# Performance work log

Hardware: AMD Instinct MI355X
Metric: run time of the kernel (lower is better)

The kernel has to match this reference:

```python
import jax, jax.numpy as jnp
import numpy as np

WIN = 5  # mask_window_size


def gather_windows(indices, image, win):
    """Gather win x win windows of pixel features centered at each query index.
    indices: [Q, 2] (y, x) int; image: [H, W, F].
    Returns keys [Q, win, win, F] (zeros at out-of-bounds) and pad mask [Q, win, win]."""
    H, W = image.shape[0], image.shape[1]
    offs = jnp.arange(win) - win // 2
    yy = (indices[:, 0, None] + offs)[:, :, None]
    xx = (indices[:, 1, None] + offs)[:, None, :]
    pad = (yy < 0) | (yy >= H) | (xx < 0) | (xx >= W)
    yc = jnp.clip(yy, 0, H - 1)
    xc = jnp.clip(xx, 0, W - 1)
    keys = image[yc, xc]
    keys = jnp.where(pad[..., None], jnp.zeros((), keys.dtype), keys)
    return keys, pad


def mlp(x, w1, b1, w2, b2):
    return jax.nn.relu(x @ w1 + b1) @ w2 + b2


def setup_inputs() -> dict:
    key = jax.random.key(0)
    ks = jax.random.split(key, 8)
    Q, Dq, F, Hd = 16384, 128, 128, 256
    H, W = 1024, 1024
    return {
        "queries": jax.random.normal(ks[0], (Q, Dq), jnp.float32),
        "query_indices": jax.random.randint(ks[1], (Q, 2), 0, H),
        "image": jax.random.normal(ks[2], (H, W, F), jnp.float32),
        "pm_w1": jax.random.normal(ks[3], (F, Hd), jnp.float32) * 0.02,
        "pm_b1": jnp.zeros((Hd,), jnp.float32),
        "pm_w2": jax.random.normal(ks[4], (Hd, Dq), jnp.float32) * 0.02,
        "pm_b2": jnp.zeros((Dq,), jnp.float32),
        "qp_w1": jax.random.normal(ks[5], (Dq, Hd), jnp.float32) * 0.02,
        "qp_b1": jnp.zeros((Hd,), jnp.float32),
        "qp_w2": jax.random.normal(ks[6], (Hd, F), jnp.float32) * 0.02,
        "qp_b2": jnp.zeros((F,), jnp.float32),
    }


def reference(queries, query_indices, image, pm_w1, pm_b1, pm_w2, pm_b2,
              qp_w1, qp_b1, qp_w2, qp_b2):
    # windowed key gather with out-of-bounds padding
    mask_keys, key_pad_mask = gather_windows(query_indices, image, WIN)  # [Q,w,w,F]
    # pixel_mask_head on gathered keys: F -> hidden -> query_dim
    mlped_mask_keys = mlp(mask_keys, pm_w1, pm_b1, pm_w2, pm_b2)          # [Q,w,w,Dq]
    binary_mask_logits = jnp.einsum('qf,qhwf->qhw', queries, mlped_mask_keys)
    # query_portion_head on queries: query_dim -> hidden -> F
    mlped_queries = mlp(queries, qp_w1, qp_b1, qp_w2, qp_b2)              # [Q,F]
    portion_logits = jnp.einsum('qf,qhwf->qhw', mlped_queries, mask_keys)
    # additive -inf pad bias (matches masked_fill + add in torch)
    pad_bias = jnp.where(key_pad_mask, -jnp.inf, 0.0).astype(binary_mask_logits.dtype)
    binary_mask_logits = binary_mask_logits + pad_bias
    portion_logits = portion_logits + pad_bias
    nonzero_key_mask = jnp.any(mask_keys != 0, axis=-1)
    return binary_mask_logits, portion_logits, nonzero_key_mask
```

## Files before the change

### kernel.cpp

```cpp
#include <hip/hip_runtime.h>
#include <math.h>

#define NEG_SENTINEL (-3.0e38f)


typedef __bf16 bf16_t;
typedef __bf16 bf16x8 __attribute__((ext_vector_type(8)));
typedef float  f32x4  __attribute__((ext_vector_type(4)));

#define MFMA(a, b, c) __builtin_amdgcn_mfma_f32_16x16x32_bf16((a), (b), (c), 0, 0, 0)

__device__ inline bf16x8 cvt_bf16x8(float4 a, float4 b) {
  bf16x8 r;
  r[0] = (bf16_t)a.x; r[1] = (bf16_t)a.y; r[2] = (bf16_t)a.z; r[3] = (bf16_t)a.w;
  r[4] = (bf16_t)b.x; r[5] = (bf16_t)b.y; r[6] = (bf16_t)b.z; r[7] = (bf16_t)b.w;
  return r;
}

__global__ __launch_bounds__(256) void prep_kernel(
    const float* __restrict__ pm_w1, const float* __restrict__ qp_w1,
    const float* __restrict__ qp_w2, const float* __restrict__ pm_w2,
    bf16_t* __restrict__ w1t, bf16_t* __restrict__ qw1t,
    bf16_t* __restrict__ qw2t, bf16_t* __restrict__ w2pm)
{
  int i = blockIdx.x * 256 + threadIdx.x;
  int m = i >> 15, e = i & 32767;
  if (m == 0)      { int n = e >> 7, k = e & 127; w1t[e]  = (bf16_t)pm_w1[k * 256 + n]; }
  else if (m == 1) { int n = e >> 7, k = e & 127; qw1t[e] = (bf16_t)qp_w1[k * 256 + n]; }
  else if (m == 2) { int f = e >> 8, h = e & 255; qw2t[e] = (bf16_t)qp_w2[h * 128 + f]; }
  else             { w2pm[e] = (bf16_t)pm_w2[e]; }
}

__global__ __launch_bounds__(256) void query_side_kernel(
    const float* __restrict__ queries,
    const float* __restrict__ pm_b2,
    const float* __restrict__ qp_b1, const float* __restrict__ qp_b2,
    const bf16_t* __restrict__ qw1t, const bf16_t* __restrict__ w2pm,
    const bf16_t* __restrict__ qw2t,
    bf16_t* __restrict__ v_ws, bf16_t* __restrict__ mq_ws, float* __restrict__ c_ws)
{
  __shared__ float qb1_lds[256];
  __shared__ float qb2_lds[128];
  __shared__ __align__(16) bf16_t hq_lds[4][4096];

  const int t = threadIdx.x;
  const int w = t >> 6, l = t & 63, lr = l & 15, lg = l >> 4;
  const int qb = blockIdx.x * 64;
  const int qrow = qb + w * 16 + lr;

  for (int i = t; i < 256; i += 256) qb1_lds[i] = qp_b1[i];
  if (t < 128) qb2_lds[t] = qp_b2[t];

  bf16x8 aq[4];
  float cpart = 0.f;
  const float* qp = queries + (size_t)qrow * 128;
  #pragma unroll
  for (int s = 0; s < 4; ++s) {
    int k0 = s * 32 + lg * 8;
    float4 u0 = *(const float4*)(qp + k0);
    float4 u1 = *(const float4*)(qp + k0 + 4);
    float4 b0 = *(const float4*)(pm_b2 + k0);
    float4 b1 = *(const float4*)(pm_b2 + k0 + 4);
    cpart += u0.x*b0.x + u0.y*b0.y + u0.z*b0.z + u0.w*b0.w
           + u1.x*b1.x + u1.y*b1.y + u1.z*b1.z + u1.w*b1.w;
    aq[s] = cvt_bf16x8(u0, u1);
  }
  cpart += __shfl_xor(cpart, 16);
  cpart += __shfl_xor(cpart, 32);
  if (l < 16) c_ws[qb + w * 16 + l] = cpart;

  __syncthreads();

  bf16_t* hqw = hq_lds[w];

  #pragma unroll 2
  for (int n = 0; n < 16; ++n) {
    f32x4 aa = {0.f, 0.f, 0.f, 0.f};
    f32x4 ac = {0.f, 0.f, 0.f, 0.f};
    const int col = n * 16 + lr;
    #pragma unroll
    for (int s = 0; s < 4; ++s) {
      bf16x8 ba = *(const bf16x8*)(qw1t + (size_t)col * 128 + (s * 4 + lg) * 8);
      bf16x8 bc = *(const bf16x8*)(w2pm + (size_t)col * 128 + (s * 4 + lg) * 8);
      aa = MFMA(aq[s], ba, aa);
      ac = MFMA(aq[s], bc, ac);
    }
    float bv = qb1_lds[col];
    const int k8 = col >> 3;
    #pragma unroll
    for (int j = 0; j < 4; ++j) {
      int rw = lg * 4 + j;
      float hv = fmaxf(aa[j] + bv, 0.f);
      hqw[rw * 256 + ((k8 ^ rw) * 8) + (col & 7)] = (bf16_t)hv;
      v_ws[(size_t)(qb + w * 16 + rw) * 256 + col] = (bf16_t)ac[j];
    }
  }

  __syncthreads();

  bf16x8 ah[8];
  #pragma unroll
  for (int s = 0; s < 8; ++s)
    ah[s] = *(const bf16x8*)(hqw + lr * 256 + (((s * 4 + lg) ^ lr) * 8));
  #pragma unroll 2
  for (int n = 0; n < 8; ++n) {
    f32x4 am = {0.f, 0.f, 0.f, 0.f};
    const int col = n * 16 + lr;
    #pragma unroll
    for (int s = 0; s < 8; ++s) {
      bf16x8 bm = *(const bf16x8*)(qw2t + (size_t)col * 256 + (s * 4 + lg) * 8);
      am = MFMA(ah[s], bm, am);
    }
    float bv = qb2_lds[col];
    #pragma unroll
    for (int j = 0; j < 4; ++j)
      mq_ws[(size_t)(qb + w * 16 + lg * 4 + j) * 128 + col] = (bf16_t)(am[j] + bv);
  }
}

__global__ __launch_bounds__(320, 2) void window_kernel(
    const int* __restrict__ qidx, const float* __restrict__ image,
    const float* __restrict__ pm_b1,
    const bf16_t* __restrict__ w1t_g,
    const bf16_t* __restrict__ v_ws, const bf16_t* __restrict__ mq_ws,
    const float* __restrict__ c_ws, float* __restrict__ out, int Q)
{
  __shared__ __align__(16) bf16x8 w1t_lds[4096];
  __shared__ __align__(16) float v_lds[16 * 256];
  __shared__ __align__(16) float mq_lds[16 * 128];
  __shared__ float b1_lds[256];
  __shared__ float c_lds[16];
  __shared__ unsigned char pad_lds[400];

  const int t = threadIdx.x;
  const int w = t >> 6, l = t & 63, lr = l & 15, lg = l >> 4;
  const int qb = blockIdx.x * 16;

  bf16x8 afr[5][4];
  int aq[5], apad[5], nzf[5];
  #pragma unroll
  for (int tt = 0; tt < 5; ++tt) {
    int r = w * 80 + tt * 16 + lr;
    int ql = r / 25;
    int cell = r - ql * 25;
    int dy = cell / 5 - 2;
    int dx = cell - (dy + 2) * 5 - 2;
    int yy = qidx[2 * (qb + ql) + 0] + dy;
    int xx = qidx[2 * (qb + ql) + 1] + dx;
    bool pad = (yy < 0) | (yy >= 1024) | (xx < 0) | (xx >= 1024);
    aq[tt] = ql; apad[tt] = pad ? 1 : 0;
    if (l < 16) pad_lds[r] = (unsigned char)(pad ? 1 : 0);
    const float* px = image + (size_t)(pad ? 0 : (yy * 1024 + xx)) * 128;
    int nz = 0;
    #pragma unroll
    for (int s = 0; s < 4; ++s) {
      float4 u0 = make_float4(0.f, 0.f, 0.f, 0.f), u1 = u0;
      if (!pad) {
        u0 = *(const float4*)(px + s * 32 + lg * 8);
        u1 = *(const float4*)(px + s * 32 + lg * 8 + 4);
      }
      nz |= (u0.x != 0.f) | (u0.y != 0.f) | (u0.z != 0.f) | (u0.w != 0.f)
          | (u1.x != 0.f) | (u1.y != 0.f) | (u1.z != 0.f) | (u1.w != 0.f);
      afr[tt][s] = cvt_bf16x8(u0, u1);
    }
    nzf[tt] = nz;
  }

  {
    const bf16x8* wg = (const bf16x8*)w1t_g;
    for (int i = t; i < 4096; i += 320) {
      int row = i >> 4, k8 = i & 15;
      w1t_lds[(row << 4) | (k8 ^ (row & 15))] = wg[i];
    }
  }
  {
    const bf16_t* vg = v_ws + (size_t)qb * 256;
    for (int i = t; i < 512; i += 320) {
      bf16x8 d = *(const bf16x8*)(vg + i * 8);
      float4 lo = make_float4((float)d[0], (float)d[1], (float)d[2], (float)d[3]);
      float4 hi = make_float4((float)d[4], (float)d[5], (float)d[6], (float)d[7]);
      *(float4*)(v_lds + i * 8) = lo;
      *(float4*)(v_lds + i * 8 + 4) = hi;
    }
  }
  {
    const bf16_t* mg = mq_ws + (size_t)qb * 128;
    for (int i = t; i < 256; i += 320) {
      bf16x8 d = *(const bf16x8*)(mg + i * 8);
      float4 lo = make_float4((float)d[0], (float)d[1], (float)d[2], (float)d[3]);
      float4 hi = make_float4((float)d[4], (float)d[5], (float)d[6], (float)d[7]);
      *(float4*)(mq_lds + i * 8) = lo;
      *(float4*)(mq_lds + i * 8 + 4) = hi;
    }
  }
  for (int i = t; i < 256; i += 320) b1_lds[i] = pm_b1[i];
  if (t < 16) c_lds[t] = c_ws[qb + t];

  __syncthreads();

  #pragma unroll
  for (int tt = 0; tt < 5; ++tt) {
    const float* mrow = mq_lds + aq[tt] * 128;
    float pp = 0.f;
    #pragma unroll
    for (int s = 0; s < 4; ++s) {
      const float* m = mrow + s * 32 + lg * 8;
      float4 m0 = *(const float4*)(m);
      float4 m1 = *(const float4*)(m + 4);
      bf16x8 a = afr[tt][s];
      pp += (float)a[0]*m0.x + (float)a[1]*m0.y + (float)a[2]*m0.z + (float)a[3]*m0.w
          + (float)a[4]*m1.x + (float)a[5]*m1.y + (float)a[6]*m1.z + (float)a[7]*m1.w;
    }
    pp += __shfl_xor(pp, 16);
    pp += __shfl_xor(pp, 32);
    int nz = nzf[tt];
    nz |= __shfl_xor(nz, 16);
    nz |= __shfl_xor(nz, 32);
    if (l < 16) {
      int r = w * 80 + tt * 16 + l;
      int ql = aq[tt];
      int cell = r - ql * 25;
      int q = qb + ql;
      out[(size_t)Q * 25 + (size_t)q * 25 + cell]     = apad[tt] ? NEG_SENTINEL : pp;
      out[(size_t)2 * Q * 25 + (size_t)q * 25 + cell] = nz ? 1.0f : 0.0f;
    }
  }

  #pragma unroll
  for (int tt = 0; tt < 5; ++tt) {
    int rcq[4], rcell[4], vb[4], pc[4];
    #pragma unroll
    for (int j = 0; j < 4; ++j) {
      int rc = w * 80 + tt * 16 + lg * 4 + j;
      int q = rc / 25;
      rcq[j] = q; rcell[j] = rc - q * 25;
      pc[j] = pad_lds[rc];
      vb[j] = q * 256 + lr;
    }
    float part[4] = {0.f, 0.f, 0.f, 0.f};
    #pragma unroll 2
    for (int n = 0; n < 16; ++n) {
      f32x4 acc = {0.f, 0.f, 0.f, 0.f};
      #pragma unroll
      for (int s = 0; s < 4; ++s) {
        bf16x8 b = w1t_lds[((n * 16 + lr) << 4) | ((s * 4 + lg) ^ lr)];
        acc = MFMA(afr[tt][s], b, acc);
      }
      float bv = b1_lds[n * 16 + lr];
      #pragma unroll
      for (int j = 0; j < 4; ++j) {
        float hv = fmaxf(acc[j] + bv, 0.f);
        part[j] = fmaf(hv, v_lds[vb[j] + n * 16], part[j]);
      }
    }
    #pragma unroll
    for (int j = 0; j < 4; ++j) {
      float s = part[j];
      s += __shfl_xor(s, 1);
      s += __shfl_xor(s, 2);
      s += __shfl_xor(s, 4);
      s += __shfl_xor(s, 8);
      if (lr == 0)
        out[(size_t)(qb + rcq[j]) * 25 + rcell[j]] =
            pc[j] ? NEG_SENTINEL : (s + c_lds[rcq[j]]);
    }
  }
}

extern "C" void kernel_launch(void* const* d_in, const int* in_sizes, int n_in,
                              void* d_out, int out_size, void* d_ws, size_t ws_size,
                              hipStream_t stream) {
  const float* queries = (const float*)d_in[0];
  const int*   qidx    = (const int*)d_in[1];
  const float* image   = (const float*)d_in[2];
  const float* pm_w1   = (const float*)d_in[3];
  const float* pm_b1   = (const float*)d_in[4];
  const float* pm_w2   = (const float*)d_in[5];
  const float* pm_b2   = (const float*)d_in[6];
  const float* qp_w1   = (const float*)d_in[7];
  const float* qp_b1   = (const float*)d_in[8];
  const float* qp_w2   = (const float*)d_in[9];
  const float* qp_b2   = (const float*)d_in[10];
  float* out = (float*)d_out;

  const int Q = in_sizes[0] / 128;

  char* ws = (char*)d_ws;
  bf16_t* v_ws  = (bf16_t*)ws;  ws += (size_t)Q * 256 * 2;
  bf16_t* mq_ws = (bf16_t*)ws;  ws += (size_t)Q * 128 * 2;
  float*  c_ws  = (float*)ws;   ws += (size_t)Q * 4;
  bf16_t* w1t   = (bf16_t*)ws;  ws += 32768 * 2;
  bf16_t* qw1t  = (bf16_t*)ws;  ws += 32768 * 2;
  bf16_t* qw2t  = (bf16_t*)ws;  ws += 32768 * 2;
  bf16_t* w2pm  = (bf16_t*)ws;  ws += 32768 * 2;

  prep_kernel<<<512, 256, 0, stream>>>(pm_w1, qp_w1, qp_w2, pm_w2,
                                       w1t, qw1t, qw2t, w2pm);
  query_side_kernel<<<Q / 64, 256, 0, stream>>>(queries, pm_b2, qp_b1, qp_b2,
                                                qw1t, w2pm, qw2t, v_ws, mq_ws, c_ws);
  window_kernel<<<Q / 16, 320, 0, stream>>>(qidx, image, pm_b1, w1t,
                                            v_ws, mq_ws, c_ws, out, Q);
}
```

Before: 745.8 us.

## Read W1 fragments from global per n-step and reuse across row tiles

Removes the 64KB LDS staging of the transposed W1 weights and instead loads each 16-column slice of W1 directly from global memory (L2/L1 cached), reusing it across all five row tiles by interchanging the tt and n loops. This frees LDS, which may allow more resident blocks, and drops the LDS fill and its read traffic. In exchange each wave issues global loads inside the MFMA loop and keeps 20 accumulators live, raising register pressure and exposing global latency.

```diff
diff --git a/kernel.cpp b/kernel.cpp
--- a/kernel.cpp
+++ b/kernel.cpp
@@ -125,7 +125,6 @@
     const bf16_t* __restrict__ v_ws, const bf16_t* __restrict__ mq_ws,
     const float* __restrict__ c_ws, float* __restrict__ out, int Q)
 {
-  __shared__ __align__(16) bf16x8 w1t_lds[4096];
   __shared__ __align__(16) float v_lds[16 * 256];
   __shared__ __align__(16) float mq_lds[16 * 128];
   __shared__ float b1_lds[256];
@@ -167,13 +166,6 @@
   }
 
   {
-    const bf16x8* wg = (const bf16x8*)w1t_g;
-    for (int i = t; i < 4096; i += 320) {
-      int row = i >> 4, k8 = i & 15;
-      w1t_lds[(row << 4) | (k8 ^ (row & 15))] = wg[i];
-    }
-  }
-  {
     const bf16_t* vg = v_ws + (size_t)qb * 256;
     for (int i = t; i < 512; i += 320) {
       bf16x8 d = *(const bf16x8*)(vg + i * 8);
@@ -226,43 +218,56 @@
     }
   }
 
+  int vb[5][4];
   #pragma unroll
   for (int tt = 0; tt < 5; ++tt) {
-    int rcq[4], rcell[4], vb[4], pc[4];
     #pragma unroll
     for (int j = 0; j < 4; ++j) {
       int rc = w * 80 + tt * 16 + lg * 4 + j;
-      int q = rc / 25;
-      rcq[j] = q; rcell[j] = rc - q * 25;
-      pc[j] = pad_lds[rc];
-      vb[j] = q * 256 + lr;
-    }
-    float part[4] = {0.f, 0.f, 0.f, 0.f};
-    #pragma unroll 2
-    for (int n = 0; n < 16; ++n) {
+      vb[tt][j] = (rc / 25) * 256 + lr;
+    }
+  }
+  float part[5][4];
+  #pragma unroll
+  for (int tt = 0; tt < 5; ++tt)
+    #pragma unroll
+    for (int j = 0; j < 4; ++j) part[tt][j] = 0.f;
+
+  #pragma unroll 2
+  for (int n = 0; n < 16; ++n) {
+    bf16x8 b[4];
+    #pragma unroll
+    for (int s = 0; s < 4; ++s)
+      b[s] = *(const bf16x8*)(w1t_g + (size_t)(n * 16 + lr) * 128 + (s * 4 + lg) * 8);
+    float bv = b1_lds[n * 16 + lr];
+    #pragma unroll
+    for (int tt = 0; tt < 5; ++tt) {
       f32x4 acc = {0.f, 0.f, 0.f, 0.f};
       #pragma unroll
-      for (int s = 0; s < 4; ++s) {
-        bf16x8 b = w1t_lds[((n * 16 + lr) << 4) | ((s * 4 + lg) ^ lr)];
-        acc = MFMA(afr[tt][s], b, acc);
-      }
-      float bv = b1_lds[n * 16 + lr];
+      for (int s = 0; s < 4; ++s) acc = MFMA(afr[tt][s], b[s], acc);
       #pragma unroll
       for (int j = 0; j < 4; ++j) {
         float hv = fmaxf(acc[j] + bv, 0.f);
-        part[j] = fmaf(hv, v_lds[vb[j] + n * 16], part[j]);
+        part[tt][j] = fmaf(hv, v_lds[vb[tt][j] + n * 16], part[tt][j]);
       }
     }
+  }
+
+  #pragma unroll
+  for (int tt = 0; tt < 5; ++tt) {
     #pragma unroll
     for (int j = 0; j < 4; ++j) {
-      float s = part[j];
+      float s = part[tt][j];
       s += __shfl_xor(s, 1);
       s += __shfl_xor(s, 2);
       s += __shfl_xor(s, 4);
       s += __shfl_xor(s, 8);
-      if (lr == 0)
-        out[(size_t)(qb + rcq[j]) * 25 + rcell[j]] =
-            pc[j] ? NEG_SENTINEL : (s + c_lds[rcq[j]]);
+      if (lr == 0) {
+        int rc = w * 80 + tt * 16 + lg * 4 + j;
+        int q = rc / 25, cell = rc - q * 25;
+        out[(size_t)(qb + q) * 25 + cell] =
+            pad_lds[rc] ? NEG_SENTINEL : (s + c_lds[q]);
+      }
     }
   }
 }
```

New measurement: 733.6 us. About the same (-1.6%).

## Cut window kernel LDS and registers, split query-side work across waves

Applied to the files above, without the earlier changes.

The window kernel stops staging the 64KB W1 tile in LDS and reads its B fragments straight from global/L2. It also stops holding all five A-fragment tiles in registers, loading each tile inside the loop, and replaces the pad LDS array with a ballot mask. Together these aim to raise occupancy (launch bounds go from 2 to 4 blocks). The query-side kernel now processes 16 queries per block with the four waves splitting output columns, which gives four times more blocks. The cost is repeated global/L2 reads of W1 per tile and less latency hiding for the image gathers, since they are no longer all issued up front.

```diff
diff --git a/kernel.cpp b/kernel.cpp
--- a/kernel.cpp
+++ b/kernel.cpp
@@ -31,7 +31,7 @@
   else             { w2pm[e] = (bf16_t)pm_w2[e]; }
 }
 
-__global__ __launch_bounds__(256) void query_side_kernel(
+__global__ __launch_bounds__(256, 4) void query_side_kernel(
     const float* __restrict__ queries,
     const float* __restrict__ pm_b2,
     const float* __restrict__ qp_b1, const float* __restrict__ qp_b2,
@@ -41,19 +41,18 @@
 {
   __shared__ float qb1_lds[256];
   __shared__ float qb2_lds[128];
-  __shared__ __align__(16) bf16_t hq_lds[4][4096];
+  __shared__ __align__(16) bf16_t hq_lds[16 * 256];
 
   const int t = threadIdx.x;
   const int w = t >> 6, l = t & 63, lr = l & 15, lg = l >> 4;
-  const int qb = blockIdx.x * 64;
-  const int qrow = qb + w * 16 + lr;
-
-  for (int i = t; i < 256; i += 256) qb1_lds[i] = qp_b1[i];
+  const int qb = blockIdx.x * 16;
+
+  qb1_lds[t] = qp_b1[t];
   if (t < 128) qb2_lds[t] = qp_b2[t];
 
   bf16x8 aq[4];
   float cpart = 0.f;
-  const float* qp = queries + (size_t)qrow * 128;
+  const float* qp = queries + (size_t)(qb + lr) * 128;
   #pragma unroll
   for (int s = 0; s < 4; ++s) {
     int k0 = s * 32 + lg * 8;
@@ -67,17 +66,15 @@
   }
   cpart += __shfl_xor(cpart, 16);
   cpart += __shfl_xor(cpart, 32);
-  if (l < 16) c_ws[qb + w * 16 + l] = cpart;
+  if (w == 0 && l < 16) c_ws[qb + l] = cpart;
 
   __syncthreads();
 
-  bf16_t* hqw = hq_lds[w];
-
-  #pragma unroll 2
-  for (int n = 0; n < 16; ++n) {
+  #pragma unroll
+  for (int n = 0; n < 4; ++n) {
     f32x4 aa = {0.f, 0.f, 0.f, 0.f};
     f32x4 ac = {0.f, 0.f, 0.f, 0.f};
-    const int col = n * 16 + lr;
+    const int col = w * 64 + n * 16 + lr;
     #pragma unroll
     for (int s = 0; s < 4; ++s) {
       bf16x8 ba = *(const bf16x8*)(qw1t + (size_t)col * 128 + (s * 4 + lg) * 8);
@@ -91,8 +88,8 @@
     for (int j = 0; j < 4; ++j) {
       int rw = lg * 4 + j;
       float hv = fmaxf(aa[j] + bv, 0.f);
-      hqw[rw * 256 + ((k8 ^ rw) * 8) + (col & 7)] = (bf16_t)hv;
-      v_ws[(size_t)(qb + w * 16 + rw) * 256 + col] = (bf16_t)ac[j];
+      hq_lds[rw * 256 + ((k8 ^ rw) * 8) + (col & 7)] = (bf16_t)hv;
+      v_ws[(size_t)(qb + rw) * 256 + col] = (bf16_t)ac[j];
     }
   }
 
@@ -101,11 +98,11 @@
   bf16x8 ah[8];
   #pragma unroll
   for (int s = 0; s < 8; ++s)
-    ah[s] = *(const bf16x8*)(hqw + lr * 256 + (((s * 4 + lg) ^ lr) * 8));
-  #pragma unroll 2
-  for (int n = 0; n < 8; ++n) {
+    ah[s] = *(const bf16x8*)(hq_lds + lr * 256 + (((s * 4 + lg) ^ lr) * 8));
+  #pragma unroll
+  for (int n = 0; n < 2; ++n) {
     f32x4 am = {0.f, 0.f, 0.f, 0.f};
-    const int col = n * 16 + lr;
+    const int col = w * 32 + n * 16 + lr;
     #pragma unroll
     for (int s = 0; s < 8; ++s) {
       bf16x8 bm = *(const bf16x8*)(qw2t + (size_t)col * 256 + (s * 4 + lg) * 8);
@@ -114,65 +111,26 @@
     float bv = qb2_lds[col];
     #pragma unroll
     for (int j = 0; j < 4; ++j)
-      mq_ws[(size_t)(qb + w * 16 + lg * 4 + j) * 128 + col] = (bf16_t)(am[j] + bv);
-  }
-}
-
-__global__ __launch_bounds__(320, 2) void window_kernel(
+      mq_ws[(size_t)(qb + lg * 4 + j) * 128 + col] = (bf16_t)(am[j] + bv);
+  }
+}
+
+__global__ __launch_bounds__(320, 4) void window_kernel(
     const int* __restrict__ qidx, const float* __restrict__ image,
     const float* __restrict__ pm_b1,
     const bf16_t* __restrict__ w1t_g,
     const bf16_t* __restrict__ v_ws, const bf16_t* __restrict__ mq_ws,
     const float* __restrict__ c_ws, float* __restrict__ out, int Q)
 {
-  __shared__ __align__(16) bf16x8 w1t_lds[4096];
   __shared__ __align__(16) float v_lds[16 * 256];
   __shared__ __align__(16) float mq_lds[16 * 128];
   __shared__ float b1_lds[256];
   __shared__ float c_lds[16];
-  __shared__ unsigned char pad_lds[400];
 
   const int t = threadIdx.x;
   const int w = t >> 6, l = t & 63, lr = l & 15, lg = l >> 4;
   const int qb = blockIdx.x * 16;
 
-  bf16x8 afr[5][4];
-  int aq[5], apad[5], nzf[5];
-  #pragma unroll
-  for (int tt = 0; tt < 5; ++tt) {
-    int r = w * 80 + tt * 16 + lr;
-    int ql = r / 25;
-    int cell = r - ql * 25;
-    int dy = cell / 5 - 2;
-    int dx = cell - (dy + 2) * 5 - 2;
-    int yy = qidx[2 * (qb + ql) + 0] + dy;
-    int xx = qidx[2 * (qb + ql) + 1] + dx;
-    bool pad = (yy < 0) | (yy >= 1024) | (xx < 0) | (xx >= 1024);
-    aq[tt] = ql; apad[tt] = pad ? 1 : 0;
-    if (l < 16) pad_lds[r] = (unsigned char)(pad ? 1 : 0);
-    const float* px = image + (size_t)(pad ? 0 : (yy * 1024 + xx)) * 128;
-    int nz = 0;
-    #pragma unroll
-    for (int s = 0; s < 4; ++s) {
-      float4 u0 = make_float4(0.f, 0.f, 0.f, 0.f), u1 = u0;
-      if (!pad) {
-        u0 = *(const float4*)(px + s * 32 + lg * 8);
-        u1 = *(const float4*)(px + s * 32 + lg * 8 + 4);
-      }
-      nz |= (u0.x != 0.f) | (u0.y != 0.f) | (u0.z != 0.f) | (u0.w != 0.f)
-          | (u1.x != 0.f) | (u1.y != 0.f) | (u1.z != 0.f) | (u1.w != 0.f);
-      afr[tt][s] = cvt_bf16x8(u0, u1);
-    }
-    nzf[tt] = nz;
-  }
-
-  {
-    const bf16x8* wg = (const bf16x8*)w1t_g;
-    for (int i = t; i < 4096; i += 320) {
-      int row = i >> 4, k8 = i & 15;
-      w1t_lds[(row << 4) | (k8 ^ (row & 15))] = wg[i];
-    }
-  }
   {
     const bf16_t* vg = v_ws + (size_t)qb * 256;
     for (int i = t; i < 512; i += 320) {
@@ -198,55 +156,75 @@
 
   __syncthreads();
 
-  #pragma unroll
+  #pragma unroll 1
   for (int tt = 0; tt < 5; ++tt) {
-    const float* mrow = mq_lds + aq[tt] * 128;
-    float pp = 0.f;
+    const int r = w * 80 + tt * 16 + lr;
+    const int ql = r / 25;
+    const int cell = r - ql * 25;
+    const int dy = cell / 5 - 2;
+    const int dx = cell - (dy + 2) * 5 - 2;
+    const int yy = qidx[2 * (qb + ql) + 0] + dy;
+    const int xx = qidx[2 * (qb + ql) + 1] + dx;
+    const bool pad = (yy < 0) | (yy >= 1024) | (xx < 0) | (xx >= 1024);
+    const float* px = image + (size_t)(pad ? 0 : (yy * 1024 + xx)) * 128;
+    bf16x8 afr[4];
+    int nz = 0;
     #pragma unroll
     for (int s = 0; s < 4; ++s) {
-      const float* m = mrow + s * 32 + lg * 8;
-      float4 m0 = *(const float4*)(m);
-      float4 m1 = *(const float4*)(m + 4);
-      bf16x8 a = afr[tt][s];
-      pp += (float)a[0]*m0.x + (float)a[1]*m0.y + (float)a[2]*m0.z + (float)a[3]*m0.w
-          + (float)a[4]*m1.x + (float)a[5]*m1.y + (float)a[6]*m1.z + (float)a[7]*m1.w;
-    }
-    pp += __shfl_xor(pp, 16);
-    pp += __shfl_xor(pp, 32);
-    int nz = nzf[tt];
-    nz |= __shfl_xor(nz, 16);
-    nz |= __shfl_xor(nz, 32);
-    if (l < 16) {
-      int r = w * 80 + tt * 16 + l;
-      int ql = aq[tt];
-      int cell = r - ql * 25;
-      int q = qb + ql;
-      out[(size_t)Q * 25 + (size_t)q * 25 + cell]     = apad[tt] ? NEG_SENTINEL : pp;
-      out[(size_t)2 * Q * 25 + (size_t)q * 25 + cell] = nz ? 1.0f : 0.0f;
-    }
-  }
-
-  #pragma unroll
-  for (int tt = 0; tt < 5; ++tt) {
-    int rcq[4], rcell[4], vb[4], pc[4];
+      float4 u0 = make_float4(0.f, 0.f, 0.f, 0.f), u1 = u0;
+      if (!pad) {
+        u0 = *(const float4*)(px + s * 32 + lg * 8);
+        u1 = *(const float4*)(px + s * 32 + lg * 8 + 4);
+      }
+      nz |= (u0.x != 0.f) | (u0.y != 0.f) | (u0.z != 0.f) | (u0.w != 0.f)
+          | (u1.x != 0.f) | (u1.y != 0.f) | (u1.z != 0.f) | (u1.w != 0.f);
+      afr[s] = cvt_bf16x8(u0, u1);
+    }
+    const unsigned long long pm = __ballot(pad);
+
+    {
+      const float* mrow = mq_lds + ql * 128;
+      float pp = 0.f;
+      #pragma unroll
+      for (int s = 0; s < 4; ++s) {
+        const float* m = mrow + s * 32 + lg * 8;
+        float4 m0 = *(const float4*)(m);
+        float4 m1 = *(const float4*)(m + 4);
+        bf16x8 a = afr[s];
+        pp += (float)a[0]*m0.x + (float)a[1]*m0.y + (float)a[2]*m0.z + (float)a[3]*m0.w
+            + (float)a[4]*m1.x + (float)a[5]*m1.y + (float)a[6]*m1.z + (float)a[7]*m1.w;
+      }
+      pp += __shfl_xor(pp, 16);
+      pp += __shfl_xor(pp, 32);
+      int nzr = nz;
+      nzr |= __shfl_xor(nzr, 16);
+      nzr |= __shfl_xor(nzr, 32);
+      if (l < 16) {
+        const int q = qb + ql;
+        out[(size_t)Q * 25 + (size_t)q * 25 + cell]     = pad ? NEG_SENTINEL : pp;
+        out[(size_t)2 * Q * 25 + (size_t)q * 25 + cell] = nzr ? 1.0f : 0.0f;
+      }
+    }
+
+    float part[4] = {0.f, 0.f, 0.f, 0.f};
+    int vb[4], rq[4], rcell[4];
     #pragma unroll
     for (int j = 0; j < 4; ++j) {
-      int rc = w * 80 + tt * 16 + lg * 4 + j;
-      int q = rc / 25;
-      rcq[j] = q; rcell[j] = rc - q * 25;
-      pc[j] = pad_lds[rc];
-      vb[j] = q * 256 + lr;
-    }
-    float part[4] = {0.f, 0.f, 0.f, 0.f};
+      const int rc = w * 80 + tt * 16 + lg * 4 + j;
+      rq[j] = rc / 25;
+      rcell[j] = rc - rq[j] * 25;
+      vb[j] = rq[j] * 256 + lr;
+    }
     #pragma unroll 2
     for (int n = 0; n < 16; ++n) {
+      bf16x8 b[4];
+      #pragma unroll
+      for (int s = 0; s < 4; ++s)
+        b[s] = *(const bf16x8*)(w1t_g + (size_t)(n * 16 + lr) * 128 + (s * 4 + lg) * 8);
       f32x4 acc = {0.f, 0.f, 0.f, 0.f};
       #pragma unroll
-      for (int s = 0; s < 4; ++s) {
-        bf16x8 b = w1t_lds[((n * 16 + lr) << 4) | ((s * 4 + lg) ^ lr)];
-        acc = MFMA(afr[tt][s], b, acc);
-      }
-      float bv = b1_lds[n * 16 + lr];
+      for (int s = 0; s < 4; ++s) acc = MFMA(afr[s], b[s], acc);
+      const float bv = b1_lds[n * 16 + lr];
       #pragma unroll
       for (int j = 0; j < 4; ++j) {
         float hv = fmaxf(acc[j] + bv, 0.f);
@@ -260,9 +238,11 @@
       s += __shfl_xor(s, 2);
       s += __shfl_xor(s, 4);
       s += __shfl_xor(s, 8);
-      if (lr == 0)
-        out[(size_t)(qb + rcq[j]) * 25 + rcell[j]] =
-            pc[j] ? NEG_SENTINEL : (s + c_lds[rcq[j]]);
+      if (lr == 0) {
+        const int rowb = lg * 4 + j;
+        out[(size_t)(qb + rq[j]) * 25 + rcell[j]] =
+            ((pm >> rowb) & 1ull) ? NEG_SENTINEL : (s + c_lds[rq[j]]);
+      }
     }
   }
 }
@@ -296,7 +276,7 @@
 
   prep_kernel<<<512, 256, 0, stream>>>(pm_w1, qp_w1, qp_w2, pm_w2,
                                        w1t, qw1t, qw2t, w2pm);
-  query_side_kernel<<<Q / 64, 256, 0, stream>>>(queries, pm_b2, qp_b1, qp_b2,
+  query_side_kernel<<<Q / 16, 256, 0, stream>>>(queries, pm_b2, qp_b1, qp_b2,
                                                 qw1t, w2pm, qw2t, v_ws, mq_ws, c_ws);
   window_kernel<<<Q / 16, 320, 0, stream>>>(qidx, image, pm_b1, w1t,
                                             v_ws, mq_ws, c_ws, out, Q);
```

After: 805.5 us. 1.08x slower.
